# Kernel tuning notes

Hardware: AMD Instinct MI355X
Metric: run time of the kernel (lower is better)

The kernel has to match this reference:

```python
import jax, jax.numpy as jnp
import numpy as np

N = 50000
E = 100000
H = 768          # hidden_size
NH = 12          # num_heads
HD = H // NH     # head dim = 64
NG = 64          # number of graphs in batch
NC = 10          # num_classes
NEG_SLOPE = 0.2


def _p(key, shape, scale=0.05):
    return jax.random.normal(key, shape, dtype=jnp.float32) * scale


def setup_inputs() -> dict:
    key = jax.random.key(0)
    ks = jax.random.split(key, 24)
    x = jax.random.normal(ks[0], (N, 3), dtype=jnp.float32)
    edge_index = jax.random.randint(ks[1], (2, E), 0, N, dtype=jnp.int32)
    batch = jnp.sort(jax.random.randint(ks[2], (N,), 0, NG, dtype=jnp.int32))
    inp = {
        'x': x, 'edge_index': edge_index, 'batch': batch,
        # GCN layers
        'w1': _p(ks[3], (3, H)), 'b1': jnp.zeros((H,), jnp.float32),
        'w2': _p(ks[4], (H, H)), 'b2': jnp.zeros((H,), jnp.float32),
        'w3': _p(ks[5], (H, H)), 'b3': jnp.zeros((H,), jnp.float32),
        # GAT layer 1
        'wg1': _p(ks[6], (H, H)), 'as1': _p(ks[7], (NH, HD)), 'ad1': _p(ks[8], (NH, HD)), 'bg1': jnp.zeros((H,), jnp.float32),
        # GAT layer 2
        'wg2': _p(ks[9], (H, H)), 'as2': _p(ks[10], (NH, HD)), 'ad2': _p(ks[11], (NH, HD)), 'bg2': jnp.zeros((H,), jnp.float32),
        # classifier MLP
        'wc1': _p(ks[12], (H, H // 2)), 'bc1': jnp.zeros((H // 2,), jnp.float32),
        'wc2': _p(ks[13], (H // 2, NC)), 'bc2': jnp.zeros((NC,), jnp.float32),
    }
    return inp


def _add_self_loops(edge_index):
    loop = jnp.arange(N, dtype=edge_index.dtype)
    src = jnp.concatenate([edge_index[0], loop])
    dst = jnp.concatenate([edge_index[1], loop])
    return src, dst


def gcn_conv(x, w, b, src, dst):
    # PyG GCNConv: self-loops + symmetric normalization D^-1/2 A D^-1/2
    h = x @ w                                   # [N, out]
    deg = jnp.zeros((N,), h.dtype).at[dst].add(1.0)   # includes self-loops -> >= 1
    dinv = jax.lax.rsqrt(deg)
    norm = (dinv[src] * dinv[dst])[:, None]     # [E', 1]
    msg = h[src] * norm                          # gather-scale
    out = jnp.zeros_like(h).at[dst].add(msg)     # scatter-add
    return out + b


def gat_conv(x, w, a_src, a_dst, b, src, dst):
    # PyG GATConv: self-loops, LeakyReLU(0.2), scatter-softmax over dst, concat heads
    h = (x @ w).reshape(N, NH, HD)
    alpha_s = jnp.einsum('nhd,hd->nh', h, a_src)  # [N, H]
    alpha_d = jnp.einsum('nhd,hd->nh', h, a_dst)
    e = jax.nn.leaky_relu(alpha_s[src] + alpha_d[dst], NEG_SLOPE)  # [E', H]
    m = jax.ops.segment_max(e, dst, num_segments=N)                 # [N, H]
    ex = jnp.exp(e - m[dst])
    s = jax.ops.segment_sum(ex, dst, num_segments=N)
    alpha = ex / s[dst]                                             # [E', H]
    out = jax.ops.segment_sum(h[src] * alpha[:, :, None], dst, num_segments=N)
    return out.reshape(N, NH * HD) + b


def global_mean_pool(x, batch):
    s = jax.ops.segment_sum(x, batch, num_segments=NG)
    cnt = jax.ops.segment_sum(jnp.ones((N,), x.dtype), batch, num_segments=NG)
    return s / jnp.maximum(cnt, 1.0)[:, None]


def reference(x, edge_index, batch, w1, b1, w2, b2, w3, b3,
              wg1, as1, ad1, bg1, wg2, as2, ad2, bg2,
              wc1, bc1, wc2, bc2):
    src, dst = _add_self_loops(edge_index)
    h = jax.nn.relu(gcn_conv(x, w1, b1, src, dst))
    # dropout is identity in eval mode
    h = jax.nn.relu(gcn_conv(h, w2, b2, src, dst))
    h = jax.nn.relu(gcn_conv(h, w3, b3, src, dst))
    h = jax.nn.relu(gat_conv(h, wg1, as1, ad1, bg1, src, dst))
    h = gat_conv(h, wg2, as2, ad2, bg2, src, dst)
    g = global_mean_pool(h, batch)                 # [NG, H]
    z = jax.nn.relu(g @ wc1 + bc1)
    logits = z @ wc2 + bc2                         # [NG, NC]
    return logits
```

## Files before the change

kernel.cpp:

```cpp
#include <hip/hip_runtime.h>
#include <math.h>

#define N_NODES 50000
#define N_EDGES 100000
#define H 768
#define NH 12
#define HD 64
#define NG 64
#define NC 10
#define H2 384
#define PCH 32
#define NSB 196

typedef _Float16 h8  __attribute__((ext_vector_type(8)));
typedef _Float16 h4v __attribute__((ext_vector_type(4)));
typedef float    ffrag __attribute__((ext_vector_type(4)));

__device__ _Float16 g_ah[(size_t)N_NODES * H];
__device__ _Float16 g_ch[(size_t)N_NODES * H];
__device__ _Float16 g_wh[4 * H * H];
__device__ float    g_dinv[N_NODES];
__device__ int      g_degi[N_NODES];
__device__ int      g_bsum[256];
__device__ int      g_boff[256];
__device__ int      g_cursor[N_NODES];
__device__ int      g_rowptr[N_NODES + 1];
__device__ int      g_csrsrc[N_EDGES];
__device__ float    g_aS[(size_t)N_NODES * NH];
__device__ float    g_aD[(size_t)N_NODES * NH];
__device__ float    g_selfc[(size_t)N_NODES * NH];
__device__ float    g_coef[(size_t)N_EDGES * NH];
__device__ float    g_ppool[(size_t)NG * PCH * H];

__device__ inline int clampi(int v, int hi) { return (v < 0) ? 0 : (v >= hi ? hi - 1 : v); }

__device__ inline void gload_lds16(const _Float16* g, _Float16* s) {
    __builtin_amdgcn_global_load_lds(
        (const __attribute__((address_space(1))) void*)g,
        (__attribute__((address_space(3))) void*)s, 16, 0, 0);
}

__global__ void fill_i32(int* p, int n, int v) {
    int i = blockIdx.x * blockDim.x + threadIdx.x;
    if (i < n) p[i] = v;
}

__global__ void count_deg(const int* __restrict__ dst, int* __restrict__ degi) {
    int e = blockIdx.x * blockDim.x + threadIdx.x;
    if (e < N_EDGES) atomicAdd(&degi[clampi(dst[e], N_NODES)], 1);
}

__global__ __launch_bounds__(256) void scan1(const int* __restrict__ degi, int* __restrict__ bsum) {
    __shared__ int s[256];
    int b = blockIdx.x, t = threadIdx.x;
    int idx = b * 256 + t;
    s[t] = (idx < N_NODES) ? degi[idx] : 0;
    __syncthreads();
    for (int off = 128; off > 0; off >>= 1) {
        if (t < off) s[t] += s[t + off];
        __syncthreads();
    }
    if (t == 0) bsum[b] = s[0];
}

__global__ __launch_bounds__(256) void scan2(const int* __restrict__ bsum, int* __restrict__ boff,
                                             int* __restrict__ rowptr) {
    __shared__ int s[256];
    int t = threadIdx.x;
    int v = (t < NSB) ? bsum[t] : 0;
    s[t] = v;
    __syncthreads();
    for (int off = 1; off < 256; off <<= 1) {
        int x = (t >= off) ? s[t - off] : 0;
        __syncthreads();
        s[t] += x;
        __syncthreads();
    }
    if (t < NSB) boff[t] = s[t] - v;
    if (t == NSB - 1) rowptr[N_NODES] = s[t];
}

__global__ __launch_bounds__(256) void scan3(const int* __restrict__ degi, const int* __restrict__ boff,
                                             int* __restrict__ rowptr, int* __restrict__ cursor,
                                             float* __restrict__ dinv) {
    __shared__ int s[256];
    int b = blockIdx.x, t = threadIdx.x;
    int idx = b * 256 + t;
    int v = (idx < N_NODES) ? degi[idx] : 0;
    s[t] = v;
    __syncthreads();
    for (int off = 1; off < 256; off <<= 1) {
        int x = (t >= off) ? s[t - off] : 0;
        __syncthreads();
        s[t] += x;
        __syncthreads();
    }
    if (idx < N_NODES) {
        int excl = s[t] - v + boff[b];
        rowptr[idx] = excl;
        cursor[idx] = excl;
        dinv[idx] = rsqrtf((float)v + 1.0f);
    }
}

__global__ void bin_edges(const int* __restrict__ src, const int* __restrict__ dst,
                          int* __restrict__ cursor, int* __restrict__ csrsrc) {
    int e = blockIdx.x * blockDim.x + threadIdx.x;
    if (e >= N_EDGES) return;
    int d = clampi(dst[e], N_NODES);
    int pos = atomicAdd(&cursor[d], 1);
    if (pos >= 0 && pos < N_EDGES) csrsrc[pos] = clampi(src[e], N_NODES);
}

__global__ void split_wT4(const float* __restrict__ w2, const float* __restrict__ w3,
                          const float* __restrict__ wg1, const float* __restrict__ wg2,
                          _Float16* __restrict__ out) {
    int idx = blockIdx.x * blockDim.x + threadIdx.x;
    if (idx >= 4 * H * H) return;
    int l = idx / (H * H), r = idx % (H * H);
    const float* w = (l == 0) ? w2 : (l == 1) ? w3 : (l == 2) ? wg1 : wg2;
    int n = r % H, k = r / H;
    out[(size_t)l * H * H + (size_t)n * H + k] = (_Float16)w[(size_t)k * H + n];
}

__global__ void gcn1_fused(const int* __restrict__ rowptr, const int* __restrict__ csrsrc,
                           const float* __restrict__ x, const float* __restrict__ dinv,
                           const float* __restrict__ w1, const float* __restrict__ b1,
                           _Float16* __restrict__ hi) {
    int d = blockIdx.x * 2 + (threadIdx.x / 96);
    int t = threadIdx.x % 96;
    if (d >= N_NODES) return;
    float dd = dinv[d];
    float c = dd * dd;
    float s0 = x[d*3] * c, s1 = x[d*3+1] * c, s2 = x[d*3+2] * c;
    int beg = rowptr[d], end = rowptr[d + 1];
    for (int i = beg; i < end; i++) {
        int s = csrsrc[i];
        float cc = dinv[s] * dd;
        s0 += x[s*3] * cc; s1 += x[s*3+1] * cc; s2 += x[s*3+2] * cc;
    }
    int j0 = t * 8;
    h8 o;
    #pragma unroll
    for (int k = 0; k < 8; k++) {
        int j = j0 + k;
        float v = s0 * w1[j] + s1 * w1[H + j] + s2 * w1[2*H + j] + b1[j];
        o[k] = (_Float16)fmaxf(v, 0.f);
    }
    ((h8*)(hi + (size_t)d * H))[t] = o;
}

__global__ __launch_bounds__(512) void gemm_f16(const _Float16* __restrict__ a,
                                                const _Float16* __restrict__ bt,
                                                _Float16* __restrict__ C, int M,
                                                const float* __restrict__ asf,
                                                const float* __restrict__ adf,
                                                float* __restrict__ aS,
                                                float* __restrict__ aD) {
    __shared__ alignas(16) _Float16 lds[3][24576];

    int tid = threadIdx.x;
    int wave = tid >> 6, lane = tid & 63;
    int quad = lane >> 4, l16 = lane & 15;
    int wm = wave >> 1, wn = wave & 1;

    int orig = blockIdx.x;
    int wgid = (orig & 7) * 147 + (orig >> 3);
    int strip = wgid / 6, colt = wgid % 6;
    int row0 = strip * 256, col0 = colt * 128;

    int lr = lane >> 3;
    int lc = lane & 7;
    int cg = lc ^ lr;
    const _Float16* gA[4];
    const _Float16* gB[2];
    int stA[4], stB[2];
    #pragma unroll
    for (int g = 0; g < 4; g++) {
        int rA = row0 + wave * 32 + g * 8 + lr;
        if (rA >= M) rA = M - 1;
        gA[g] = a + (size_t)rA * H + cg * 8;
        stA[g] = (wave * 32 + g * 8) * 64;
    }
    #pragma unroll
    for (int g = 0; g < 2; g++) {
        int rB = col0 + wave * 16 + g * 8 + lr;
        gB[g] = bt + (size_t)rB * H + cg * 8;
        stB[g] = 16384 + (wave * 16 + g * 8) * 64;
    }

    int swz = l16 & 7;
    int offA[4][2], offB[4][2];
    #pragma unroll
    for (int i = 0; i < 4; i++)
        #pragma unroll
        for (int kk = 0; kk < 2; kk++) {
            offA[i][kk] = (wm * 64 + i * 16 + l16) * 64 + (((kk * 4 + quad) ^ swz) * 8);
            offB[i][kk] = 16384 + (wn * 64 + i * 16 + l16) * 64 + (((kk * 4 + quad) ^ swz) * 8);
        }

    ffrag acc[4][4];
    #pragma unroll
    for (int i = 0; i < 4; i++)
        #pragma unroll
        for (int j = 0; j < 4; j++) { ffrag z = {0.f, 0.f, 0.f, 0.f}; acc[i][j] = z; }

    _Float16* p0 = &lds[0][0];
    _Float16* p1 = &lds[1][0];
    _Float16* p2 = &lds[2][0];

    #pragma unroll
    for (int g = 0; g < 4; g++) gload_lds16(gA[g], p0 + stA[g]);
    #pragma unroll
    for (int g = 0; g < 2; g++) gload_lds16(gB[g], p0 + stB[g]);
    #pragma unroll
    for (int g = 0; g < 4; g++) gload_lds16(gA[g] + 64, p1 + stA[g]);
    #pragma unroll
    for (int g = 0; g < 2; g++) gload_lds16(gB[g] + 64, p1 + stB[g]);
    asm volatile("s_waitcnt vmcnt(6)" ::: "memory");
    __builtin_amdgcn_s_barrier();
    asm volatile("" ::: "memory");

    _Float16 *pc = p0, *pn = p1, *pf = p2;
    #pragma unroll 1
    for (int kt = 0; kt < H / 64; kt++) {
        if (kt < H / 64 - 2) {
            #pragma unroll
            for (int g = 0; g < 4; g++) gload_lds16(gA[g] + (kt + 2) * 64, pf + stA[g]);
        }
        h8 fb[4][2], fa[2][2];
        #pragma unroll
        for (int j = 0; j < 4; j++)
            #pragma unroll
            for (int kk = 0; kk < 2; kk++)
                fb[j][kk] = *reinterpret_cast<const h8*>(pc + offB[j][kk]);
        #pragma unroll
        for (int i = 0; i < 2; i++)
            #pragma unroll
            for (int kk = 0; kk < 2; kk++)
                fa[i][kk] = *reinterpret_cast<const h8*>(pc + offA[i][kk]);
        __builtin_amdgcn_s_setprio(1);
        #pragma unroll
        for (int kk = 0; kk < 2; kk++)
            #pragma unroll
            for (int i = 0; i < 2; i++)
                #pragma unroll
                for (int j = 0; j < 4; j++)
                    acc[i][j] = __builtin_amdgcn_mfma_f32_16x16x32_f16(fa[i][kk], fb[j][kk], acc[i][j], 0, 0, 0);
        __builtin_amdgcn_s_setprio(0);
        asm volatile("s_waitcnt lgkmcnt(0)" ::: "memory");
        __builtin_amdgcn_sched_barrier(0);
        __builtin_amdgcn_s_barrier();
        asm volatile("" ::: "memory");
        if (kt < H / 64 - 2) {
            #pragma unroll
            for (int g = 0; g < 2; g++) gload_lds16(gB[g] + (kt + 2) * 64, pf + stB[g]);
        }
        h8 fa2[2][2];
        #pragma unroll
        for (int i = 0; i < 2; i++)
            #pragma unroll
            for (int kk = 0; kk < 2; kk++)
                fa2[i][kk] = *reinterpret_cast<const h8*>(pc + offA[2 + i][kk]);
        __builtin_amdgcn_s_setprio(1);
        #pragma unroll
        for (int kk = 0; kk < 2; kk++)
            #pragma unroll
            for (int i = 0; i < 2; i++)
                #pragma unroll
                for (int j = 0; j < 4; j++)
                    acc[2 + i][j] = __builtin_amdgcn_mfma_f32_16x16x32_f16(fa2[i][kk], fb[j][kk], acc[2 + i][j], 0, 0, 0);
        __builtin_amdgcn_s_setprio(0);
        asm volatile("s_waitcnt lgkmcnt(0)" ::: "memory");
        __builtin_amdgcn_sched_barrier(0);
        if (kt < H / 64 - 2) asm volatile("s_waitcnt vmcnt(6)" ::: "memory");
        else                 asm volatile("s_waitcnt vmcnt(0)" ::: "memory");
        __builtin_amdgcn_s_barrier();
        asm volatile("" ::: "memory");
        _Float16* t = pc; pc = pn; pn = pf; pf = t;
    }

    #pragma unroll
    for (int i = 0; i < 4; i++)
        #pragma unroll
        for (int r = 0; r < 4; r++) {
            int row = row0 + wm * 64 + i * 16 + quad * 4 + r;
            if (row >= M) continue;
            #pragma unroll
            for (int j = 0; j < 4; j++)
                C[(size_t)row * H + col0 + wn * 64 + j * 16 + l16] = (_Float16)acc[i][j][r];
        }

    if (asf) {
        int head = (col0 + wn * 64) >> 6;
        float as_c[4], ad_c[4];
        #pragma unroll
        for (int j = 0; j < 4; j++) {
            int col = col0 + wn * 64 + j * 16 + l16;
            as_c[j] = asf[col];
            ad_c[j] = adf[col];
        }
        #pragma unroll
        for (int i = 0; i < 4; i++)
            #pragma unroll
            for (int r = 0; r < 4; r++) {
                float ps = 0.f, pd = 0.f;
                #pragma unroll
                for (int j = 0; j < 4; j++) {
                    ps += acc[i][j][r] * as_c[j];
                    pd += acc[i][j][r] * ad_c[j];
                }
                ps += __shfl_xor(ps, 1);  pd += __shfl_xor(pd, 1);
                ps += __shfl_xor(ps, 2);  pd += __shfl_xor(pd, 2);
                ps += __shfl_xor(ps, 4);  pd += __shfl_xor(pd, 4);
                ps += __shfl_xor(ps, 8);  pd += __shfl_xor(pd, 8);
                int row = row0 + wm * 64 + i * 16 + quad * 4 + r;
                if (l16 == 0 && row < M) {
                    aS[row * NH + head] = ps;
                    aD[row * NH + head] = pd;
                }
            }
    }
}

__global__ void gcn_gather(const int* __restrict__ rowptr, const int* __restrict__ csrsrc,
                           const _Float16* __restrict__ h, const float* __restrict__ dinv,
                           const float* __restrict__ bias, _Float16* __restrict__ hi) {
    int d = blockIdx.x * 2 + (threadIdx.x / 96);
    int t = threadIdx.x % 96;
    if (d >= N_NODES) return;
    float dd = dinv[d];
    float c = dd * dd;
    h8 v = ((const h8*)(h + (size_t)d * H))[t];
    float acc[8];
    #pragma unroll
    for (int k = 0; k < 8; k++) acc[k] = (float)v[k] * c;
    int beg = rowptr[d], end = rowptr[d + 1];
    for (int i = beg; i < end; i++) {
        int s = csrsrc[i];
        float cc = dinv[s] * dd;
        h8 u = ((const h8*)(h + (size_t)s * H))[t];
        #pragma unroll
        for (int k = 0; k < 8; k++) acc[k] += (float)u[k] * cc;
    }
    float4 b0 = ((const float4*)bias)[2 * t];
    float4 b1 = ((const float4*)bias)[2 * t + 1];
    h8 o;
    o[0] = (_Float16)fmaxf(acc[0] + b0.x, 0.f);
    o[1] = (_Float16)fmaxf(acc[1] + b0.y, 0.f);
    o[2] = (_Float16)fmaxf(acc[2] + b0.z, 0.f);
    o[3] = (_Float16)fmaxf(acc[3] + b0.w, 0.f);
    o[4] = (_Float16)fmaxf(acc[4] + b1.x, 0.f);
    o[5] = (_Float16)fmaxf(acc[5] + b1.y, 0.f);
    o[6] = (_Float16)fmaxf(acc[6] + b1.z, 0.f);
    o[7] = (_Float16)fmaxf(acc[7] + b1.w, 0.f);
    ((h8*)(hi + (size_t)d * H))[t] = o;
}

__device__ inline float lrelu(float v) { return (v > 0.f) ? v : 0.2f * v; }

__global__ void gat_stats(const int* __restrict__ rowptr, const int* __restrict__ csrsrc,
                          const float* __restrict__ aS, const float* __restrict__ aD,
                          float* __restrict__ selfc, float* __restrict__ coef) {
    int idx = blockIdx.x * blockDim.x + threadIdx.x;
    if (idx >= N_NODES * NH) return;
    int d = idx / NH, hh = idx % NH;
    int beg = rowptr[d], end = rowptr[d + 1];
    float adv = aD[idx];
    float eself = lrelu(aS[idx] + adv);
    float m = eself;
    for (int i = beg; i < end; i++)
        m = fmaxf(m, lrelu(aS[csrsrc[i] * NH + hh] + adv));
    float ssum = __expf(eself - m);
    for (int i = beg; i < end; i++)
        ssum += __expf(lrelu(aS[csrsrc[i] * NH + hh] + adv) - m);
    float inv = 1.0f / ssum;
    selfc[idx] = __expf(eself - m) * inv;
    for (int i = beg; i < end; i++)
        coef[(size_t)i * NH + hh] = __expf(lrelu(aS[csrsrc[i] * NH + hh] + adv) - m) * inv;
}

__global__ void gat_gather(const int* __restrict__ rowptr, const int* __restrict__ csrsrc,
                           const _Float16* __restrict__ h, const float* __restrict__ selfc,
                           const float* __restrict__ coef, const float* __restrict__ bias,
                           _Float16* __restrict__ hi, int relu) {
    int d = blockIdx.x * 2 + (threadIdx.x / 96);
    int t = threadIdx.x % 96;
    if (d >= N_NODES) return;
    int hh = t >> 3;
    int beg = rowptr[d], end = rowptr[d + 1];
    float cself = selfc[d * NH + hh];
    h8 v = ((const h8*)(h + (size_t)d * H))[t];
    float acc[8];
    #pragma unroll
    for (int k = 0; k < 8; k++) acc[k] = (float)v[k] * cself;
    for (int i = beg; i < end; i++) {
        int s = csrsrc[i];
        float c = coef[(size_t)i * NH + hh];
        h8 u = ((const h8*)(h + (size_t)s * H))[t];
        #pragma unroll
        for (int k = 0; k < 8; k++) acc[k] += (float)u[k] * c;
    }
    float4 b0 = ((const float4*)bias)[2 * t];
    float4 b1 = ((const float4*)bias)[2 * t + 1];
    acc[0] += b0.x; acc[1] += b0.y; acc[2] += b0.z; acc[3] += b0.w;
    acc[4] += b1.x; acc[5] += b1.y; acc[6] += b1.z; acc[7] += b1.w;
    if (relu) {
        #pragma unroll
        for (int k = 0; k < 8; k++) acc[k] = fmaxf(acc[k], 0.f);
    }
    h8 o;
    #pragma unroll
    for (int k = 0; k < 8; k++) o[k] = (_Float16)acc[k];
    ((h8*)(hi + (size_t)d * H))[t] = o;
}

__device__ inline int lower_bound_i(const int* b, int n, int key) {
    int lo = 0, hi = n;
    while (lo < hi) { int mid = (lo + hi) >> 1; if (b[mid] < key) lo = mid + 1; else hi = mid; }
    return lo;
}

__global__ void pool_partial(const int* __restrict__ batch, const _Float16* __restrict__ h,
                             float* __restrict__ ppool) {
    int g = blockIdx.x / PCH, c = blockIdx.x % PCH;
    int t = threadIdx.x;
    int lo = lower_bound_i(batch, N_NODES, g);
    int hi = lower_bound_i(batch, N_NODES, g + 1);
    int len = hi - lo;
    int chunk = (len + PCH - 1) / PCH;
    int s = lo + c * chunk;
    int e = s + chunk; if (e > hi) e = hi;
    float4 a = {0, 0, 0, 0};
    for (int n = s; n < e; n++) {
        h4v v = ((const h4v*)(h + (size_t)n * H))[t];
        a.x += (float)v[0]; a.y += (float)v[1]; a.z += (float)v[2]; a.w += (float)v[3];
    }
    ((float4*)(ppool + (size_t)blockIdx.x * H))[t] = a;
}

__global__ __launch_bounds__(384) void pool_mlp(const int* __restrict__ batch,
                                                const float* __restrict__ ppool,
                                                const float* __restrict__ wc1,
                                                const float* __restrict__ bc1,
                                                const float* __restrict__ wc2,
                                                const float* __restrict__ bc2,
                                                float* __restrict__ out) {
    __shared__ float row[H];
    __shared__ float z[H2];
    int g = blockIdx.x, t = threadIdx.x;
    int lo = lower_bound_i(batch, N_NODES, g);
    int hi = lower_bound_i(batch, N_NODES, g + 1);
    float inv = 1.0f / fmaxf((float)(hi - lo), 1.0f);
    for (int c0 = t; c0 < H; c0 += 384) {
        float a = 0.f;
        for (int c = 0; c < PCH; c++) a += ppool[(size_t)(g * PCH + c) * H + c0];
        row[c0] = a * inv;
    }
    __syncthreads();
    float acc = bc1[t];
    for (int k = 0; k < H; k++) acc += row[k] * wc1[(size_t)k * H2 + t];
    z[t] = fmaxf(acc, 0.f);
    __syncthreads();
    if (t < NC) {
        float l = bc2[t];
        for (int k = 0; k < H2; k++) l += z[k] * wc2[(size_t)k * NC + t];
        out[g * NC + t] = l;
    }
}

extern "C" void kernel_launch(void* const* d_in, const int* in_sizes, int n_in,
                              void* d_out, int out_size, void* d_ws, size_t ws_size,
                              hipStream_t stream) {
    (void)d_ws; (void)ws_size;
    const float* x     = (const float*)d_in[0];
    const int*   ei    = (const int*)d_in[1];
    const int*   batch = (const int*)d_in[2];
    const float* w1  = (const float*)d_in[3];  const float* b1  = (const float*)d_in[4];
    const float* w2  = (const float*)d_in[5];  const float* b2  = (const float*)d_in[6];
    const float* w3  = (const float*)d_in[7];  const float* b3  = (const float*)d_in[8];
    const float* wg1 = (const float*)d_in[9];  const float* as1 = (const float*)d_in[10];
    const float* ad1 = (const float*)d_in[11]; const float* bg1 = (const float*)d_in[12];
    const float* wg2 = (const float*)d_in[13]; const float* as2 = (const float*)d_in[14];
    const float* ad2 = (const float*)d_in[15]; const float* bg2 = (const float*)d_in[16];
    const float* wc1 = (const float*)d_in[17]; const float* bc1 = (const float*)d_in[18];
    const float* wc2 = (const float*)d_in[19]; const float* bc2 = (const float*)d_in[20];

    const int* srcp = ei;
    const int* dstp = ei + N_EDGES;

    float *dinv, *aS, *aD, *selfc, *coef, *ppool;
    _Float16 *ah, *ch, *wh;
    int *degi, *bsum, *boff, *cursor, *rowptr, *csrsrc;
    hipGetSymbolAddress((void**)&ah,     HIP_SYMBOL(g_ah));
    hipGetSymbolAddress((void**)&ch,     HIP_SYMBOL(g_ch));
    hipGetSymbolAddress((void**)&wh,     HIP_SYMBOL(g_wh));
    hipGetSymbolAddress((void**)&dinv,   HIP_SYMBOL(g_dinv));
    hipGetSymbolAddress((void**)&degi,   HIP_SYMBOL(g_degi));
    hipGetSymbolAddress((void**)&bsum,   HIP_SYMBOL(g_bsum));
    hipGetSymbolAddress((void**)&boff,   HIP_SYMBOL(g_boff));
    hipGetSymbolAddress((void**)&cursor, HIP_SYMBOL(g_cursor));
    hipGetSymbolAddress((void**)&rowptr, HIP_SYMBOL(g_rowptr));
    hipGetSymbolAddress((void**)&csrsrc, HIP_SYMBOL(g_csrsrc));
    hipGetSymbolAddress((void**)&aS,     HIP_SYMBOL(g_aS));
    hipGetSymbolAddress((void**)&aD,     HIP_SYMBOL(g_aD));
    hipGetSymbolAddress((void**)&selfc,  HIP_SYMBOL(g_selfc));
    hipGetSymbolAddress((void**)&coef,   HIP_SYMBOL(g_coef));
    hipGetSymbolAddress((void**)&ppool,  HIP_SYMBOL(g_ppool));

    auto cdiv = [](int a, int b) { return (a + b - 1) / b; };
    int ggrid = cdiv(N_NODES, 256) * (H / 128);
    int ngath = cdiv(N_NODES, 2);
    size_t HH = (size_t)H * H;

    split_wT4<<<cdiv(4*H*H,256),256,0,stream>>>(w2, w3, wg1, wg2, wh);

    fill_i32<<<cdiv(N_NODES,256),256,0,stream>>>(degi, N_NODES, 0);
    count_deg<<<cdiv(N_EDGES,256),256,0,stream>>>(dstp, degi);
    scan1<<<NSB,256,0,stream>>>(degi, bsum);
    scan2<<<1,256,0,stream>>>(bsum, boff, rowptr);
    scan3<<<NSB,256,0,stream>>>(degi, boff, rowptr, cursor, dinv);
    bin_edges<<<cdiv(N_EDGES,256),256,0,stream>>>(srcp, dstp, cursor, csrsrc);

    gcn1_fused<<<ngath,192,0,stream>>>(rowptr, csrsrc, x, dinv, w1, b1, ah);

    gemm_f16<<<ggrid,512,0,stream>>>(ah, wh + 0*HH, ch, N_NODES,
                                     (const float*)nullptr, (const float*)nullptr,
                                     (float*)nullptr, (float*)nullptr);
    gcn_gather<<<ngath,192,0,stream>>>(rowptr, csrsrc, ch, dinv, b2, ah);

    gemm_f16<<<ggrid,512,0,stream>>>(ah, wh + 1*HH, ch, N_NODES,
                                     (const float*)nullptr, (const float*)nullptr,
                                     (float*)nullptr, (float*)nullptr);
    gcn_gather<<<ngath,192,0,stream>>>(rowptr, csrsrc, ch, dinv, b3, ah);

    gemm_f16<<<ggrid,512,0,stream>>>(ah, wh + 2*HH, ch, N_NODES, as1, ad1, aS, aD);
    gat_stats<<<cdiv(N_NODES*NH,256),256,0,stream>>>(rowptr, csrsrc, aS, aD, selfc, coef);
    gat_gather<<<ngath,192,0,stream>>>(rowptr, csrsrc, ch, selfc, coef, bg1, ah, 1);

    gemm_f16<<<ggrid,512,0,stream>>>(ah, wh + 3*HH, ch, N_NODES, as2, ad2, aS, aD);
    gat_stats<<<cdiv(N_NODES*NH,256),256,0,stream>>>(rowptr, csrsrc, aS, aD, selfc, coef);
    gat_gather<<<ngath,192,0,stream>>>(rowptr, csrsrc, ch, selfc, coef, bg2, ah, 0);

    pool_partial<<<NG*PCH,192,0,stream>>>(batch, ah, ppool);
    pool_mlp<<<NG,384,0,stream>>>(batch, ppool, wc1, bc1, wc2, bc2, (float*)d_out);
}
```

Measured before the change: 858.0 us.

## Restructure GEMM main loop into register double-buffered, two-k-tile unrolled pipeline

```diff
diff --git a/kernel.cpp b/kernel.cpp
--- a/kernel.cpp
+++ b/kernel.cpp
@@ -217,67 +217,93 @@
     for (int g = 0; g < 4; g++) gload_lds16(gA[g] + 64, p1 + stA[g]);
     #pragma unroll
     for (int g = 0; g < 2; g++) gload_lds16(gB[g] + 64, p1 + stB[g]);
+    #pragma unroll
+    for (int g = 0; g < 4; g++) gload_lds16(gA[g] + 128, p2 + stA[g]);
+    #pragma unroll
+    for (int g = 0; g < 2; g++) gload_lds16(gB[g] + 128, p2 + stB[g]);
     asm volatile("s_waitcnt vmcnt(6)" ::: "memory");
     __builtin_amdgcn_s_barrier();
-    asm volatile("" ::: "memory");
-
-    _Float16 *pc = p0, *pn = p1, *pf = p2;
+
+    h8 a0[4][2], b0[4][2], a1[4][2], b1[4][2];
+
+    #pragma unroll
+    for (int i = 0; i < 4; i++)
+        #pragma unroll
+        for (int kk = 0; kk < 2; kk++) a0[i][kk] = *reinterpret_cast<const h8*>(p0 + offA[i][kk]);
+    #pragma unroll
+    for (int j = 0; j < 4; j++)
+        #pragma unroll
+        for (int kk = 0; kk < 2; kk++) b0[j][kk] = *reinterpret_cast<const h8*>(p0 + offB[j][kk]);
+    asm volatile("s_waitcnt lgkmcnt(0)" ::: "memory");
+    __builtin_amdgcn_s_barrier();
+
+    _Float16 *pA = p0, *pB = p1, *pC = p2;
+
     #pragma unroll 1
-    for (int kt = 0; kt < H / 64; kt++) {
-        if (kt < H / 64 - 2) {
-            #pragma unroll
-            for (int g = 0; g < 4; g++) gload_lds16(gA[g] + (kt + 2) * 64, pf + stA[g]);
-        }
-        h8 fb[4][2], fa[2][2];
+    for (int ktp = 0; ktp < 6; ktp++) {
+        if (ktp <= 4) {
+            int koff = (2 * ktp + 3) * 64;
+            #pragma unroll
+            for (int g = 0; g < 4; g++) gload_lds16(gA[g] + koff, pA + stA[g]);
+            #pragma unroll
+            for (int g = 0; g < 2; g++) gload_lds16(gB[g] + koff, pA + stB[g]);
+        }
+        #pragma unroll
+        for (int i = 0; i < 4; i++)
+            #pragma unroll
+            for (int kk = 0; kk < 2; kk++) a1[i][kk] = *reinterpret_cast<const h8*>(pB + offA[i][kk]);
         #pragma unroll
         for (int j = 0; j < 4; j++)
             #pragma unroll
-            for (int kk = 0; kk < 2; kk++)
-                fb[j][kk] = *reinterpret_cast<const h8*>(pc + offB[j][kk]);
-        #pragma unroll
-        for (int i = 0; i < 2; i++)
-            #pragma unroll
-            for (int kk = 0; kk < 2; kk++)
-                fa[i][kk] = *reinterpret_cast<const h8*>(pc + offA[i][kk]);
+            for (int kk = 0; kk < 2; kk++) b1[j][kk] = *reinterpret_cast<const h8*>(pB + offB[j][kk]);
         __builtin_amdgcn_s_setprio(1);
         #pragma unroll
         for (int kk = 0; kk < 2; kk++)
             #pragma unroll
-            for (int i = 0; i < 2; i++)
+            for (int i = 0; i < 4; i++)
                 #pragma unroll
                 for (int j = 0; j < 4; j++)
-                    acc[i][j] = __builtin_amdgcn_mfma_f32_16x16x32_f16(fa[i][kk], fb[j][kk], acc[i][j], 0, 0, 0);
+                    acc[i][j] = __builtin_amdgcn_mfma_f32_16x16x32_f16(a0[i][kk], b0[j][kk], acc[i][j], 0, 0, 0);
         __builtin_amdgcn_s_setprio(0);
         asm volatile("s_waitcnt lgkmcnt(0)" ::: "memory");
-        __builtin_amdgcn_sched_barrier(0);
+        if (ktp <= 4) asm volatile("s_waitcnt vmcnt(6)" ::: "memory");
+        else          asm volatile("s_waitcnt vmcnt(0)" ::: "memory");
         __builtin_amdgcn_s_barrier();
-        asm volatile("" ::: "memory");
-        if (kt < H / 64 - 2) {
-            #pragma unroll
-            for (int g = 0; g < 2; g++) gload_lds16(gB[g] + (kt + 2) * 64, pf + stB[g]);
-        }
-        h8 fa2[2][2];
-        #pragma unroll
-        for (int i = 0; i < 2; i++)
-            #pragma unroll
-            for (int kk = 0; kk < 2; kk++)
-                fa2[i][kk] = *reinterpret_cast<const h8*>(pc + offA[2 + i][kk]);
+        { _Float16* t = pA; pA = pB; pB = pC; pC = t; }
+
+        if (ktp <= 3) {
+            int koff = (2 * ktp + 4) * 64;
+            #pragma unroll
+            for (int g = 0; g < 4; g++) gload_lds16(gA[g] + koff, pA + stA[g]);
+            #pragma unroll
+            for (int g = 0; g < 2; g++) gload_lds16(gB[g] + koff, pA + stB[g]);
+        }
+        if (ktp <= 4) {
+            #pragma unroll
+            for (int i = 0; i < 4; i++)
+                #pragma unroll
+                for (int kk = 0; kk < 2; kk++) a0[i][kk] = *reinterpret_cast<const h8*>(pB + offA[i][kk]);
+            #pragma unroll
+            for (int j = 0; j < 4; j++)
+                #pragma unroll
+                for (int kk = 0; kk < 2; kk++) b0[j][kk] = *reinterpret_cast<const h8*>(pB + offB[j][kk]);
+        }
         __builtin_amdgcn_s_setprio(1);
         #pragma unroll
         for (int kk = 0; kk < 2; kk++)
             #pragma unroll
-            for (int i = 0; i < 2; i++)
+            for (int i = 0; i < 4; i++)
                 #pragma unroll
                 for (int j = 0; j < 4; j++)
-                    acc[2 + i][j] = __builtin_amdgcn_mfma_f32_16x16x32_f16(fa2[i][kk], fb[j][kk], acc[2 + i][j], 0, 0, 0);
+                    acc[i][j] = __builtin_amdgcn_mfma_f32_16x16x32_f16(a1[i][kk], b1[j][kk], acc[i][j], 0, 0, 0);
         __builtin_amdgcn_s_setprio(0);
-        asm volatile("s_waitcnt lgkmcnt(0)" ::: "memory");
-        __builtin_amdgcn_sched_barrier(0);
-        if (kt < H / 64 - 2) asm volatile("s_waitcnt vmcnt(6)" ::: "memory");
-        else                 asm volatile("s_waitcnt vmcnt(0)" ::: "memory");
-        __builtin_amdgcn_s_barrier();
-        asm volatile("" ::: "memory");
-        _Float16* t = pc; pc = pn; pn = pf; pf = t;
+        if (ktp <= 4) {
+            asm volatile("s_waitcnt lgkmcnt(0)" ::: "memory");
+            if (ktp <= 3) asm volatile("s_waitcnt vmcnt(6)" ::: "memory");
+            else          asm volatile("s_waitcnt vmcnt(0)" ::: "memory");
+            __builtin_amdgcn_s_barrier();
+        }
+        { _Float16* t = pA; pA = pB; pB = pC; pC = t; }
     }
 
     #pragma unroll
```

Result: faster. 838.2 us (-2.3%).

## Restructure GEMM main loop to interleave LDS reads, prefetch issue and barriers

Applied to the files above, without the earlier changes.

```diff
diff --git a/kernel.cpp b/kernel.cpp
--- a/kernel.cpp
+++ b/kernel.cpp
@@ -150,13 +150,13 @@
     ((h8*)(hi + (size_t)d * H))[t] = o;
 }
 
-__global__ __launch_bounds__(512) void gemm_f16(const _Float16* __restrict__ a,
-                                                const _Float16* __restrict__ bt,
-                                                _Float16* __restrict__ C, int M,
-                                                const float* __restrict__ asf,
-                                                const float* __restrict__ adf,
-                                                float* __restrict__ aS,
-                                                float* __restrict__ aD) {
+__global__ __launch_bounds__(512, 2) void gemm_f16(const _Float16* __restrict__ a,
+                                                   const _Float16* __restrict__ bt,
+                                                   _Float16* __restrict__ C, int M,
+                                                   const float* __restrict__ asf,
+                                                   const float* __restrict__ adf,
+                                                   float* __restrict__ aS,
+                                                   float* __restrict__ aD) {
     __shared__ alignas(16) _Float16 lds[3][24576];
 
     int tid = threadIdx.x;
@@ -219,26 +219,29 @@
     for (int g = 0; g < 2; g++) gload_lds16(gB[g] + 64, p1 + stB[g]);
     asm volatile("s_waitcnt vmcnt(6)" ::: "memory");
     __builtin_amdgcn_s_barrier();
-    asm volatile("" ::: "memory");
-
-    _Float16 *pc = p0, *pn = p1, *pf = p2;
+
+    _Float16 *pc = p0, *pn = p1, *ps = p2;
+
     #pragma unroll 1
     for (int kt = 0; kt < H / 64; kt++) {
-        if (kt < H / 64 - 2) {
-            #pragma unroll
-            for (int g = 0; g < 4; g++) gload_lds16(gA[g] + (kt + 2) * 64, pf + stA[g]);
+        h8 fa0[2][2], fa1[2][2], fb[4][2];
+        #pragma unroll
+        for (int i = 0; i < 2; i++)
+            #pragma unroll
+            for (int kk = 0; kk < 2; kk++) fa0[i][kk] = *reinterpret_cast<const h8*>(pc + offA[i][kk]);
+        #pragma unroll
+        for (int j = 0; j < 4; j++)
+            #pragma unroll
+            for (int kk = 0; kk < 2; kk++) fb[j][kk] = *reinterpret_cast<const h8*>(pc + offB[j][kk]);
+        if (kt <= 9) {
+            int koff = (kt + 2) * 64;
+            #pragma unroll
+            for (int g = 0; g < 3; g++) gload_lds16(gA[g] + koff, ps + stA[g]);
         }
-        h8 fb[4][2], fa[2][2];
-        #pragma unroll
-        for (int j = 0; j < 4; j++)
-            #pragma unroll
-            for (int kk = 0; kk < 2; kk++)
-                fb[j][kk] = *reinterpret_cast<const h8*>(pc + offB[j][kk]);
-        #pragma unroll
-        for (int i = 0; i < 2; i++)
-            #pragma unroll
-            for (int kk = 0; kk < 2; kk++)
-                fa[i][kk] = *reinterpret_cast<const h8*>(pc + offA[i][kk]);
+        __builtin_amdgcn_sched_barrier(0);
+        __builtin_amdgcn_s_barrier();
+        asm volatile("s_waitcnt lgkmcnt(0)" ::: "memory");
+        __builtin_amdgcn_sched_barrier(0);
         __builtin_amdgcn_s_setprio(1);
         #pragma unroll
         for (int kk = 0; kk < 2; kk++)
@@ -246,22 +249,23 @@
             for (int i = 0; i < 2; i++)
                 #pragma unroll
                 for (int j = 0; j < 4; j++)
-                    acc[i][j] = __builtin_amdgcn_mfma_f32_16x16x32_f16(fa[i][kk], fb[j][kk], acc[i][j], 0, 0, 0);
+                    acc[i][j] = __builtin_amdgcn_mfma_f32_16x16x32_f16(fa0[i][kk], fb[j][kk], acc[i][j], 0, 0, 0);
         __builtin_amdgcn_s_setprio(0);
+
+        #pragma unroll
+        for (int i = 0; i < 2; i++)
+            #pragma unroll
+            for (int kk = 0; kk < 2; kk++) fa1[i][kk] = *reinterpret_cast<const h8*>(pc + offA[2 + i][kk]);
+        if (kt <= 9) {
+            int koff = (kt + 2) * 64;
+            gload_lds16(gA[3] + koff, ps + stA[3]);
+            #pragma unroll
+            for (int g = 0; g < 2; g++) gload_lds16(gB[g] + koff, ps + stB[g]);
+        }
+        __builtin_amdgcn_sched_barrier(0);
+        __builtin_amdgcn_s_barrier();
         asm volatile("s_waitcnt lgkmcnt(0)" ::: "memory");
         __builtin_amdgcn_sched_barrier(0);
-        __builtin_amdgcn_s_barrier();
-        asm volatile("" ::: "memory");
-        if (kt < H / 64 - 2) {
-            #pragma unroll
-            for (int g = 0; g < 2; g++) gload_lds16(gB[g] + (kt + 2) * 64, pf + stB[g]);
-        }
-        h8 fa2[2][2];
-        #pragma unroll
-        for (int i = 0; i < 2; i++)
-            #pragma unroll
-            for (int kk = 0; kk < 2; kk++)
-                fa2[i][kk] = *reinterpret_cast<const h8*>(pc + offA[2 + i][kk]);
         __builtin_amdgcn_s_setprio(1);
         #pragma unroll
         for (int kk = 0; kk < 2; kk++)
@@ -269,15 +273,16 @@
             for (int i = 0; i < 2; i++)
                 #pragma unroll
                 for (int j = 0; j < 4; j++)
-                    acc[2 + i][j] = __builtin_amdgcn_mfma_f32_16x16x32_f16(fa2[i][kk], fb[j][kk], acc[2 + i][j], 0, 0, 0);
+                    acc[2 + i][j] = __builtin_amdgcn_mfma_f32_16x16x32_f16(fa1[i][kk], fb[j][kk], acc[2 + i][j], 0, 0, 0);
         __builtin_amdgcn_s_setprio(0);
-        asm volatile("s_waitcnt lgkmcnt(0)" ::: "memory");
-        __builtin_amdgcn_sched_barrier(0);
-        if (kt < H / 64 - 2) asm volatile("s_waitcnt vmcnt(6)" ::: "memory");
-        else                 asm volatile("s_waitcnt vmcnt(0)" ::: "memory");
-        __builtin_amdgcn_s_barrier();
-        asm volatile("" ::: "memory");
-        _Float16* t = pc; pc = pn; pn = pf; pf = t;
+
+        if (kt <= 10) {
+            if (kt <= 9) asm volatile("s_waitcnt vmcnt(6)" ::: "memory");
+            else         asm volatile("s_waitcnt vmcnt(0)" ::: "memory");
+            __builtin_amdgcn_sched_barrier(0);
+            __builtin_amdgcn_s_barrier();
+        }
+        { _Float16* t = pc; pc = pn; pn = ps; ps = t; }
     }
 
     #pragma unroll
@@ -304,19 +309,19 @@
         for (int i = 0; i < 4; i++)
             #pragma unroll
             for (int r = 0; r < 4; r++) {
-                float ps = 0.f, pd = 0.f;
+                float ps2 = 0.f, pd = 0.f;
                 #pragma unroll
                 for (int j = 0; j < 4; j++) {
-                    ps += acc[i][j][r] * as_c[j];
-                    pd += acc[i][j][r] * ad_c[j];
+                    ps2 += acc[i][j][r] * as_c[j];
+                    pd  += acc[i][j][r] * ad_c[j];
                 }
-                ps += __shfl_xor(ps, 1);  pd += __shfl_xor(pd, 1);
-                ps += __shfl_xor(ps, 2);  pd += __shfl_xor(pd, 2);
-                ps += __shfl_xor(ps, 4);  pd += __shfl_xor(pd, 4);
-                ps += __shfl_xor(ps, 8);  pd += __shfl_xor(pd, 8);
+                ps2 += __shfl_xor(ps2, 1);  pd += __shfl_xor(pd, 1);
+                ps2 += __shfl_xor(ps2, 2);  pd += __shfl_xor(pd, 2);
+                ps2 += __shfl_xor(ps2, 4);  pd += __shfl_xor(pd, 4);
+                ps2 += __shfl_xor(ps2, 8);  pd += __shfl_xor(pd, 8);
                 int row = row0 + wm * 64 + i * 16 + quad * 4 + r;
                 if (l16 == 0 && row < M) {
-                    aS[row * NH + head] = ps;
+                    aS[row * NH + head] = ps2;
                     aD[row * NH + head] = pd;
                 }
             }
```

New measurement: 851.4 us. No clear change (-0.8%).

## Enlarge GEMM tile to 256x256 with half-tile staged double-buffer pipeline

Applied to the files above, without the earlier changes.

```diff
diff --git a/kernel.cpp b/kernel.cpp
--- a/kernel.cpp
+++ b/kernel.cpp
@@ -150,158 +150,187 @@
     ((h8*)(hi + (size_t)d * H))[t] = o;
 }
 
-__global__ __launch_bounds__(512) void gemm_f16(const _Float16* __restrict__ a,
-                                                const _Float16* __restrict__ bt,
-                                                _Float16* __restrict__ C, int M,
-                                                const float* __restrict__ asf,
-                                                const float* __restrict__ adf,
-                                                float* __restrict__ aS,
-                                                float* __restrict__ aD) {
-    __shared__ alignas(16) _Float16 lds[3][24576];
+__device__ inline void stageA_half(const _Float16* __restrict__ a, _Float16* lds,
+                                   int row0, int M, int wave, int lr, int cg,
+                                   int d, int h, int s) {
+    _Float16* base = lds + (d * 2 + h) * 8192;
+    #pragma unroll
+    for (int g = 0; g < 2; g++) {
+        int r = row0 + h * 128 + g * 64 + wave * 8 + lr;
+        if (r >= M) r = M - 1;
+        gload_lds16(a + (size_t)r * H + s * 64 + cg * 8, base + (g * 64 + wave * 8) * 64);
+    }
+}
+__device__ inline void stageB_half(const _Float16* __restrict__ bt, _Float16* lds,
+                                   int col0, int wave, int lr, int cg,
+                                   int d, int h, int s) {
+    _Float16* base = lds + 32768 + (d * 2 + h) * 8192;
+    #pragma unroll
+    for (int g = 0; g < 2; g++) {
+        int r = col0 + h * 128 + g * 64 + wave * 8 + lr;
+        gload_lds16(bt + (size_t)r * H + s * 64 + cg * 8, base + (g * 64 + wave * 8) * 64);
+    }
+}
+
+__global__ __launch_bounds__(512, 2) void gemm_f16(const _Float16* __restrict__ a,
+                                                   const _Float16* __restrict__ bt,
+                                                   _Float16* __restrict__ C, int M,
+                                                   const float* __restrict__ asf,
+                                                   const float* __restrict__ adf,
+                                                   float* __restrict__ aS,
+                                                   float* __restrict__ aD) {
+    __shared__ alignas(16) _Float16 lds[65536];
 
     int tid = threadIdx.x;
     int wave = tid >> 6, lane = tid & 63;
     int quad = lane >> 4, l16 = lane & 15;
-    int wm = wave >> 1, wn = wave & 1;
-
-    int orig = blockIdx.x;
-    int wgid = (orig & 7) * 147 + (orig >> 3);
-    int strip = wgid / 6, colt = wgid % 6;
-    int row0 = strip * 256, col0 = colt * 128;
+    int wm = wave >> 2, wn = wave & 3;
+
+    int strip = blockIdx.x / 3, colt = blockIdx.x % 3;
+    int row0 = strip * 256, col0 = colt * 256;
+    int cw = col0 + wn * 64;
 
     int lr = lane >> 3;
-    int lc = lane & 7;
-    int cg = lc ^ lr;
-    const _Float16* gA[4];
-    const _Float16* gB[2];
-    int stA[4], stB[2];
-    #pragma unroll
-    for (int g = 0; g < 4; g++) {
-        int rA = row0 + wave * 32 + g * 8 + lr;
-        if (rA >= M) rA = M - 1;
-        gA[g] = a + (size_t)rA * H + cg * 8;
-        stA[g] = (wave * 32 + g * 8) * 64;
-    }
-    #pragma unroll
-    for (int g = 0; g < 2; g++) {
-        int rB = col0 + wave * 16 + g * 8 + lr;
-        gB[g] = bt + (size_t)rB * H + cg * 8;
-        stB[g] = 16384 + (wave * 16 + g * 8) * 64;
-    }
+    int cg = (lane & 7) ^ lr;
 
     int swz = l16 & 7;
-    int offA[4][2], offB[4][2];
-    #pragma unroll
-    for (int i = 0; i < 4; i++)
-        #pragma unroll
-        for (int kk = 0; kk < 2; kk++) {
-            offA[i][kk] = (wm * 64 + i * 16 + l16) * 64 + (((kk * 4 + quad) ^ swz) * 8);
-            offB[i][kk] = 16384 + (wn * 64 + i * 16 + l16) * 64 + (((kk * 4 + quad) ^ swz) * 8);
+    int cx0 = (quad ^ swz) * 8;
+    int cx1 = ((4 + quad) ^ swz) * 8;
+
+    ffrag acc[8][4];
+    #pragma unroll
+    for (int i = 0; i < 8; i++)
+        #pragma unroll
+        for (int j = 0; j < 4; j++) { ffrag z = {0.f, 0.f, 0.f, 0.f}; acc[i][j] = z; }
+
+    stageA_half(a, lds, row0, M, wave, lr, cg, 0, 0, 0);
+    stageB_half(bt, lds, col0, wave, lr, cg, 0, 0, 0);
+    stageB_half(bt, lds, col0, wave, lr, cg, 0, 1, 0);
+    stageA_half(a, lds, row0, M, wave, lr, cg, 0, 1, 0);
+    stageB_half(bt, lds, col0, wave, lr, cg, 1, 0, 1);
+    stageB_half(bt, lds, col0, wave, lr, cg, 1, 1, 1);
+    asm volatile("s_waitcnt vmcnt(4)" ::: "memory");
+    __builtin_amdgcn_s_barrier();
+
+    #pragma unroll 1
+    for (int t = 0; t < 12; t++) {
+        int d = t & 1;
+        const _Float16* pA = lds + (d * 2 + wm) * 8192;
+        const _Float16* pB = lds + 32768 + (d * 2 + (wn >> 1)) * 8192;
+        int brow = (wn & 1) * 64;
+
+        h8 fa[4][2], fb0[2][2], fb1[2][2];
+
+        #pragma unroll
+        for (int i = 0; i < 4; i++) {
+            fa[i][0] = *reinterpret_cast<const h8*>(pA + (i * 16 + l16) * 64 + cx0);
+            fa[i][1] = *reinterpret_cast<const h8*>(pA + (i * 16 + l16) * 64 + cx1);
         }
-
-    ffrag acc[4][4];
-    #pragma unroll
-    for (int i = 0; i < 4; i++)
-        #pragma unroll
-        for (int j = 0; j < 4; j++) { ffrag z = {0.f, 0.f, 0.f, 0.f}; acc[i][j] = z; }
-
-    _Float16* p0 = &lds[0][0];
-    _Float16* p1 = &lds[1][0];
-    _Float16* p2 = &lds[2][0];
-
-    #pragma unroll
-    for (int g = 0; g < 4; g++) gload_lds16(gA[g], p0 + stA[g]);
-    #pragma unroll
-    for (int g = 0; g < 2; g++) gload_lds16(gB[g], p0 + stB[g]);
-    #pragma unroll
-    for (int g = 0; g < 4; g++) gload_lds16(gA[g] + 64, p1 + stA[g]);
-    #pragma unroll
-    for (int g = 0; g < 2; g++) gload_lds16(gB[g] + 64, p1 + stB[g]);
-    asm volatile("s_waitcnt vmcnt(6)" ::: "memory");
-    __builtin_amdgcn_s_barrier();
-    asm volatile("" ::: "memory");
-
-    _Float16 *pc = p0, *pn = p1, *pf = p2;
-    #pragma unroll 1
-    for (int kt = 0; kt < H / 64; kt++) {
-        if (kt < H / 64 - 2) {
-            #pragma unroll
-            for (int g = 0; g < 4; g++) gload_lds16(gA[g] + (kt + 2) * 64, pf + stA[g]);
+        #pragma unroll
+        for (int j = 0; j < 2; j++) {
+            fb0[j][0] = *reinterpret_cast<const h8*>(pB + (brow + j * 16 + l16) * 64 + cx0);
+            fb0[j][1] = *reinterpret_cast<const h8*>(pB + (brow + j * 16 + l16) * 64 + cx1);
         }
-        h8 fb[4][2], fa[2][2];
-        #pragma unroll
-        for (int j = 0; j < 4; j++)
-            #pragma unroll
-            for (int kk = 0; kk < 2; kk++)
-                fb[j][kk] = *reinterpret_cast<const h8*>(pc + offB[j][kk]);
-        #pragma unroll
-        for (int i = 0; i < 2; i++)
-            #pragma unroll
-            for (int kk = 0; kk < 2; kk++)
-                fa[i][kk] = *reinterpret_cast<const h8*>(pc + offA[i][kk]);
+        if (t <= 10) stageA_half(a, lds, row0, M, wave, lr, cg, (t + 1) & 1, 0, t + 1);
+        __builtin_amdgcn_sched_barrier(0);
+        __builtin_amdgcn_s_barrier();
+        asm volatile("s_waitcnt lgkmcnt(0)" ::: "memory");
+        __builtin_amdgcn_sched_barrier(0);
         __builtin_amdgcn_s_setprio(1);
         #pragma unroll
         for (int kk = 0; kk < 2; kk++)
             #pragma unroll
-            for (int i = 0; i < 2; i++)
+            for (int i = 0; i < 4; i++)
                 #pragma unroll
-                for (int j = 0; j < 4; j++)
-                    acc[i][j] = __builtin_amdgcn_mfma_f32_16x16x32_f16(fa[i][kk], fb[j][kk], acc[i][j], 0, 0, 0);
+                for (int j = 0; j < 2; j++)
+                    acc[i][j] = __builtin_amdgcn_mfma_f32_16x16x32_f16(fa[i][kk], fb0[j][kk], acc[i][j], 0, 0, 0);
         __builtin_amdgcn_s_setprio(0);
+        __builtin_amdgcn_sched_barrier(0);
+        __builtin_amdgcn_s_barrier();
+
+        #pragma unroll
+        for (int j = 0; j < 2; j++) {
+            fb1[j][0] = *reinterpret_cast<const h8*>(pB + (brow + (2 + j) * 16 + l16) * 64 + cx0);
+            fb1[j][1] = *reinterpret_cast<const h8*>(pB + (brow + (2 + j) * 16 + l16) * 64 + cx1);
+        }
+        if (t <= 10) stageA_half(a, lds, row0, M, wave, lr, cg, (t + 1) & 1, 1, t + 1);
+        __builtin_amdgcn_sched_barrier(0);
+        __builtin_amdgcn_s_barrier();
         asm volatile("s_waitcnt lgkmcnt(0)" ::: "memory");
         __builtin_amdgcn_sched_barrier(0);
-        __builtin_amdgcn_s_barrier();
-        asm volatile("" ::: "memory");
-        if (kt < H / 64 - 2) {
-            #pragma unroll
-            for (int g = 0; g < 2; g++) gload_lds16(gB[g] + (kt + 2) * 64, pf + stB[g]);
-        }
-        h8 fa2[2][2];
-        #pragma unroll
-        for (int i = 0; i < 2; i++)
-            #pragma unroll
-            for (int kk = 0; kk < 2; kk++)
-                fa2[i][kk] = *reinterpret_cast<const h8*>(pc + offA[2 + i][kk]);
         __builtin_amdgcn_s_setprio(1);
         #pragma unroll
         for (int kk = 0; kk < 2; kk++)
             #pragma unroll
-            for (int i = 0; i < 2; i++)
+            for (int i = 0; i < 4; i++)
                 #pragma unroll
-                for (int j = 0; j < 4; j++)
-                    acc[2 + i][j] = __builtin_amdgcn_mfma_f32_16x16x32_f16(fa2[i][kk], fb[j][kk], acc[2 + i][j], 0, 0, 0);
+                for (int j = 0; j < 2; j++)
+                    acc[i][2 + j] = __builtin_amdgcn_mfma_f32_16x16x32_f16(fa[i][kk], fb1[j][kk], acc[i][2 + j], 0, 0, 0);
         __builtin_amdgcn_s_setprio(0);
+        __builtin_amdgcn_sched_barrier(0);
+        __builtin_amdgcn_s_barrier();
+
+        #pragma unroll
+        for (int i = 0; i < 4; i++) {
+            fa[i][0] = *reinterpret_cast<const h8*>(pA + ((4 + i) * 16 + l16) * 64 + cx0);
+            fa[i][1] = *reinterpret_cast<const h8*>(pA + ((4 + i) * 16 + l16) * 64 + cx1);
+        }
+        if (t <= 9) stageB_half(bt, lds, col0, wave, lr, cg, d, 0, t + 2);
+        __builtin_amdgcn_sched_barrier(0);
+        __builtin_amdgcn_s_barrier();
         asm volatile("s_waitcnt lgkmcnt(0)" ::: "memory");
         __builtin_amdgcn_sched_barrier(0);
-        if (kt < H / 64 - 2) asm volatile("s_waitcnt vmcnt(6)" ::: "memory");
-        else                 asm volatile("s_waitcnt vmcnt(0)" ::: "memory");
-        __builtin_amdgcn_s_barrier();
-        asm volatile("" ::: "memory");
-        _Float16* t = pc; pc = pn; pn = pf; pf = t;
-    }
-
-    #pragma unroll
-    for (int i = 0; i < 4; i++)
+        __builtin_amdgcn_s_setprio(1);
+        #pragma unroll
+        for (int kk = 0; kk < 2; kk++)
+            #pragma unroll
+            for (int i = 0; i < 4; i++)
+                #pragma unroll
+                for (int j = 0; j < 2; j++)
+                    acc[4 + i][2 + j] = __builtin_amdgcn_mfma_f32_16x16x32_f16(fa[i][kk], fb1[j][kk], acc[4 + i][2 + j], 0, 0, 0);
+        __builtin_amdgcn_s_setprio(0);
+        __builtin_amdgcn_sched_barrier(0);
+        __builtin_amdgcn_s_barrier();
+
+        if (t <= 9) stageB_half(bt, lds, col0, wave, lr, cg, d, 1, t + 2);
+        __builtin_amdgcn_sched_barrier(0);
+        __builtin_amdgcn_s_barrier();
+        __builtin_amdgcn_s_setprio(1);
+        #pragma unroll
+        for (int kk = 0; kk < 2; kk++)
+            #pragma unroll
+            for (int i = 0; i < 4; i++)
+                #pragma unroll
+                for (int j = 0; j < 2; j++)
+                    acc[4 + i][j] = __builtin_amdgcn_mfma_f32_16x16x32_f16(fa[i][kk], fb0[j][kk], acc[4 + i][j], 0, 0, 0);
+        __builtin_amdgcn_s_setprio(0);
+        if (t <= 9)       asm volatile("s_waitcnt vmcnt(4)" ::: "memory");
+        else if (t == 10) asm volatile("s_waitcnt vmcnt(0)" ::: "memory");
+        __builtin_amdgcn_sched_barrier(0);
+        __builtin_amdgcn_s_barrier();
+    }
+
+    #pragma unroll
+    for (int i = 0; i < 8; i++)
         #pragma unroll
         for (int r = 0; r < 4; r++) {
-            int row = row0 + wm * 64 + i * 16 + quad * 4 + r;
+            int row = row0 + wm * 128 + i * 16 + quad * 4 + r;
             if (row >= M) continue;
             #pragma unroll
             for (int j = 0; j < 4; j++)
-                C[(size_t)row * H + col0 + wn * 64 + j * 16 + l16] = (_Float16)acc[i][j][r];
+                C[(size_t)row * H + cw + j * 16 + l16] = (_Float16)acc[i][j][r];
         }
 
     if (asf) {
-        int head = (col0 + wn * 64) >> 6;
+        int head = colt * 4 + wn;
         float as_c[4], ad_c[4];
         #pragma unroll
         for (int j = 0; j < 4; j++) {
-            int col = col0 + wn * 64 + j * 16 + l16;
-            as_c[j] = asf[col];
-            ad_c[j] = adf[col];
+            as_c[j] = asf[cw + j * 16 + l16];
+            ad_c[j] = adf[cw + j * 16 + l16];
         }
         #pragma unroll
-        for (int i = 0; i < 4; i++)
+        for (int i = 0; i < 8; i++)
             #pragma unroll
             for (int r = 0; r < 4; r++) {
                 float ps = 0.f, pd = 0.f;
@@ -314,7 +343,7 @@
                 ps += __shfl_xor(ps, 2);  pd += __shfl_xor(pd, 2);
                 ps += __shfl_xor(ps, 4);  pd += __shfl_xor(pd, 4);
                 ps += __shfl_xor(ps, 8);  pd += __shfl_xor(pd, 8);
-                int row = row0 + wm * 64 + i * 16 + quad * 4 + r;
+                int row = row0 + wm * 128 + i * 16 + quad * 4 + r;
                 if (l16 == 0 && row < M) {
                     aS[row * NH + head] = ps;
                     aD[row * NH + head] = pd;
@@ -509,7 +538,7 @@
     hipGetSymbolAddress((void**)&ppool,  HIP_SYMBOL(g_ppool));
 
     auto cdiv = [](int a, int b) { return (a + b - 1) / b; };
-    int ggrid = cdiv(N_NODES, 256) * (H / 128);
+    int ggrid = cdiv(N_NODES, 256) * (H / 256);
     int ngath = cdiv(N_NODES, 2);
     size_t HH = (size_t)H * H;
 
```

Measured after the change: 857.5 us. No clear change (-0.1%).
